# Kernel tuning notes

Hardware: AMD Instinct MI355X
Metric: run time of the kernel (lower is better)

Reference implementation:

```python
import jax, jax.numpy as jnp
import numpy as np

H = 100  # hidden size
T_ENC, T_DEC = 12, 50


def setup_inputs() -> dict:
    key = jax.random.key(0)
    ks = iter(jax.random.split(key, 40))
    n = lambda *s: jax.random.normal(next(ks), s, dtype=jnp.float32) * 0.1
    B = 16384
    inp = {
        "q": jax.random.normal(next(ks), (B, T_ENC, H), dtype=jnp.float32),
        "p": jax.random.normal(next(ks), (B, T_DEC, H), dtype=jnp.float32),
        # attention
        "attn_W": n(H, H), "attn_b": n(H),
        # encoder GRU (2 layers, input 100)
        "eWih0": n(3 * H, H), "eWhh0": n(3 * H, H), "ebih0": n(3 * H), "ebhh0": n(3 * H),
        "eWih1": n(3 * H, H), "eWhh1": n(3 * H, H), "ebih1": n(3 * H), "ebhh1": n(3 * H),
        # decoder GRU (2 layers, layer0 input 200)
        "dWih0": n(3 * H, 2 * H), "dWhh0": n(3 * H, H), "dbih0": n(3 * H), "dbhh0": n(3 * H),
        "dWih1": n(3 * H, H), "dWhh1": n(3 * H, H), "dbih1": n(3 * H), "dbhh1": n(3 * H),
        # out_context Linear(200,50)
        "outW": n(50, 2 * H), "outb": n(50),
        # final MLP 50->25->10->4->2
        "f1W": n(25, 50), "f1b": n(25),
        "f2W": n(10, 25), "f2b": n(10),
        "f3W": n(4, 10), "f3b": n(4),
        "f4W": n(2, 4), "f4b": n(2),
    }
    return inp


def _gru_cell(x, h, Wih, Whh, bih, bhh):
    gi = x @ Wih.T + bih
    gh = h @ Whh.T + bhh
    ir, iz, inn = jnp.split(gi, 3, axis=-1)
    hr, hz, hn = jnp.split(gh, 3, axis=-1)
    r = jax.nn.sigmoid(ir + hr)
    z = jax.nn.sigmoid(iz + hz)
    ng = jnp.tanh(inn + r * hn)
    return (1.0 - z) * ng + z * h


def reference(q, p, attn_W, attn_b,
              eWih0, eWhh0, ebih0, ebhh0, eWih1, eWhh1, ebih1, ebhh1,
              dWih0, dWhh0, dbih0, dbhh0, dWih1, dWhh1, dbih1, dbhh1,
              outW, outb, f1W, f1b, f2W, f2b, f3W, f3b, f4W, f4b):
    B = q.shape[0]
    h_init = jnp.zeros((B, H), q.dtype)

    # encoder: 2-layer GRU over 12 timesteps
    def enc_step(carry, xt):
        h0, h1 = carry
        h0 = _gru_cell(xt, h0, eWih0, eWhh0, ebih0, ebhh0)
        h1 = _gru_cell(h0, h1, eWih1, eWhh1, ebih1, ebhh1)
        return (h0, h1), h1

    (h0, h1), enc_seq = jax.lax.scan(enc_step, (h_init, h_init), jnp.swapaxes(q, 0, 1))
    enc = jnp.swapaxes(enc_seq, 0, 1)  # [B, 12, H]

    # precompute attn energies: Linear(H,H) applied to encoder outputs
    energy = jnp.einsum("btd,ed->bte", enc, attn_W) + attn_b  # [B, 12, H]

    # decoder: 50 steps of attention + 2-layer GRU + out_context
    def dec_step(carry, xt):
        h0, h1 = carry
        scores = jnp.einsum("bd,btd->bt", h1, energy)  # hidden = last layer
        aw = jax.nn.softmax(scores, axis=1)
        ctx = jnp.einsum("bt,btd->bd", aw, enc)  # [B, H]
        gin = jnp.concatenate([xt, ctx], axis=-1)  # [B, 2H]
        h0 = _gru_cell(gin, h0, dWih0, dWhh0, dbih0, dbhh0)
        h1 = _gru_cell(h0, h1, dWih1, dWhh1, dbih1, dbhh1)
        out = jax.nn.relu(jnp.concatenate([h1, ctx], axis=1) @ outW.T + outb)
        return (h0, h1), out

    _, outs = jax.lax.scan(dec_step, (h0, h1), jnp.swapaxes(p, 0, 1))
    s = outs[-1]  # [B, 50]

    s = jax.nn.relu(s @ f1W.T + f1b)
    s = jax.nn.relu(s @ f2W.T + f2b)
    s = jax.nn.relu(s @ f3W.T + f3b)
    return jax.nn.softmax(s @ f4W.T + f4b, axis=1)
```

## Files before the change

### kernel.cpp

```cpp
#include <hip/hip_runtime.h>


#define BB    16384
#define HH    100
#define TE    12
#define TDN   50
#define ROWS  64
#define XS    101
#define GS    205
#define ENCT_OFF 16384

struct Params {
  const float *q, *p, *attn_b;
  const float *eWih0,*eWhh0,*ebih0,*ebhh0,*eWih1,*eWhh1,*ebih1,*ebhh1;
  const float *dWih0,*dWhh0,*dbih0,*dbhh0,*dWih1,*dWhh1,*dbih1,*dbhh1;
  const float *outW,*outb,*f1W,*f1b,*f2W,*f2b,*f3W,*f3b,*f4W,*f4b;
  float *ws;
  float *out;
};

__global__ void prep_attn_t(const float* __restrict__ attn_W, float* __restrict__ ws) {
  int i = blockIdx.x * 256 + threadIdx.x;
  if (i < HH * HH) {
    int d = i / HH, e = i % HH;
    ws[d * HH + e] = attn_W[e * HH + d];
  }
}

__device__ __forceinline__ float sigf(float x)   { return 1.0f / (1.0f + __expf(-x)); }
__device__ __forceinline__ float tanhf_(float x) { float e = __expf(2.0f * x); return 1.0f - 2.0f / (e + 1.0f); }

template<int NG, int K, int LDW>
__device__ __forceinline__ void gemm_sw(const float* __restrict__ W,
                                        const float* xrow, int wv, float* acc) {
  #pragma unroll
  for (int m = 0; m < NG; ++m) acc[m] = 0.0f;
  #pragma unroll 1
  for (int kc = 0; kc < K; kc += 25) {
    float xr[25];
    #pragma unroll
    for (int i = 0; i < 25; ++i) xr[i] = xrow[kc + i];
    #pragma unroll
    for (int m = 0; m < NG; ++m) {
      const float* wr = W + (wv + 4 * m) * LDW + kc;
      float a = acc[m];
      #pragma unroll
      for (int i = 0; i < 25; ++i) a = fmaf(wr[i], xr[i], a);
      acc[m] = a;
    }
  }
}

template<bool WRITE_ENC>
__device__ __forceinline__ void gru_combine(const float* gi, const float* gh,
    const float* __restrict__ bih, const float* __restrict__ bhh,
    int wv, int lane, float (*hS)[XS], float* __restrict__ encT, int grow) {
  #pragma unroll
  for (int m = 0; m < 25; ++m) {
    const int n = wv + 4 * m;
    float ir  = gi[m]      + bih[n];
    float iz  = gi[m + 25] + bih[n + 100];
    float inn = gi[m + 50] + bih[n + 200];
    float hr  = gh[m]      + bhh[n];
    float hz  = gh[m + 25] + bhh[n + 100];
    float hn  = gh[m + 50] + bhh[n + 200];
    float r  = sigf(ir + hr);
    float z  = sigf(iz + hz);
    float ng = tanhf_(inn + r * hn);
    float hp = hS[lane][n];
    float hv = (1.0f - z) * ng + z * hp;
    hS[lane][n] = hv;
    if (WRITE_ENC) encT[n * BB + grow] = hv;
  }
}

__global__ __launch_bounds__(256, 1) void fused_kernel(Params pr) {
  __shared__ float h0s[ROWS][XS];
  __shared__ float h1s[ROWS][XS];
  __shared__ float xb [ROWS][GS];
  __shared__ float gvb[ROWS][XS];
  __shared__ float scb[ROWS][13];
  __shared__ float ob [ROWS][53];

  const int tid  = threadIdx.x;
  const int lane = tid & 63;
  const int wv   = __builtin_amdgcn_readfirstlane(tid >> 6);
  const int r0   = blockIdx.x * ROWS;
  const int grow = r0 + lane;

  for (int it = tid; it < ROWS * XS; it += 256) {
    (&h0s[0][0])[it] = 0.0f;
    (&h1s[0][0])[it] = 0.0f;
  }
  __syncthreads();

  float gi[75], gh[75];

  for (int t = 0; t < TE; ++t) {
    for (int it = tid; it < ROWS * HH; it += 256) {
      int r = it / HH, k = it % HH;
      xb[r][k] = pr.q[(size_t)(r0 + r) * (TE * HH) + t * HH + k];
    }
    __syncthreads();
    gemm_sw<75, 100, 100>(pr.eWih0, &xb[lane][0],  wv, gi);
    gemm_sw<75, 100, 100>(pr.eWhh0, &h0s[lane][0], wv, gh);
    __syncthreads();
    gru_combine<false>(gi, gh, pr.ebih0, pr.ebhh0, wv, lane, h0s, nullptr, grow);
    __syncthreads();
    gemm_sw<75, 100, 100>(pr.eWih1, &h0s[lane][0], wv, gi);
    gemm_sw<75, 100, 100>(pr.eWhh1, &h1s[lane][0], wv, gh);
    __syncthreads();
    gru_combine<true>(gi, gh, pr.ebih1, pr.ebhh1, wv, lane, h1s,
                      pr.ws + ENCT_OFF + (size_t)t * HH * BB, grow);
    __syncthreads();
  }

  const float* encT  = pr.ws + ENCT_OFF;
  const float* attnT = pr.ws;

  for (int t = 0; t < TDN; ++t) {
    {
      float ga[25];
      gemm_sw<25, 100, 100>(attnT, &h1s[lane][0], wv, ga);
      #pragma unroll
      for (int m = 0; m < 25; ++m) gvb[lane][wv + 4 * m] = ga[m];
    }
    float cb = 0.0f;
    #pragma unroll 4
    for (int e = 0; e < HH; ++e) cb = fmaf(h1s[lane][e], pr.attn_b[e], cb);
    __syncthreads();

    {
      const int tb = 3 * wv;
      float sc0 = cb, sc1 = cb, sc2 = cb;
      #pragma unroll 1
      for (int dc = 0; dc < HH; dc += 25) {
        float gv[25];
        #pragma unroll
        for (int i = 0; i < 25; ++i) gv[i] = gvb[lane][dc + i];
        #pragma unroll
        for (int i = 0; i < 25; ++i) {
          sc0 = fmaf(gv[i], encT[(size_t)((tb + 0) * HH + dc + i) * BB + grow], sc0);
          sc1 = fmaf(gv[i], encT[(size_t)((tb + 1) * HH + dc + i) * BB + grow], sc1);
          sc2 = fmaf(gv[i], encT[(size_t)((tb + 2) * HH + dc + i) * BB + grow], sc2);
        }
      }
      scb[lane][tb + 0] = sc0;
      scb[lane][tb + 1] = sc1;
      scb[lane][tb + 2] = sc2;
    }
    __syncthreads();

    float aw[TE];
    {
      float mx = -1e30f;
      #pragma unroll
      for (int k = 0; k < TE; ++k) { float v = scb[lane][k]; aw[k] = v; mx = fmaxf(mx, v); }
      float s = 0.0f;
      #pragma unroll
      for (int k = 0; k < TE; ++k) { float e = __expf(aw[k] - mx); aw[k] = e; s += e; }
      float inv = 1.0f / s;
      #pragma unroll
      for (int k = 0; k < TE; ++k) aw[k] *= inv;
    }

    {
      const int db = 25 * wv;
      float cx[25];
      #pragma unroll
      for (int i = 0; i < 25; ++i) cx[i] = 0.0f;
      #pragma unroll
      for (int k = 0; k < TE; ++k) {
        float a = aw[k];
        #pragma unroll
        for (int i = 0; i < 25; ++i)
          cx[i] = fmaf(a, encT[(size_t)(k * HH + db + i) * BB + grow], cx[i]);
      }
      #pragma unroll
      for (int i = 0; i < 25; ++i) xb[lane][HH + db + i] = cx[i];
    }
    for (int it = tid; it < ROWS * HH; it += 256) {
      int r = it / HH, k = it % HH;
      xb[r][k] = pr.p[(size_t)(r0 + r) * (TDN * HH) + t * HH + k];
    }
    __syncthreads();

    gemm_sw<75, 200, 200>(pr.dWih0, &xb[lane][0],  wv, gi);
    gemm_sw<75, 100, 100>(pr.dWhh0, &h0s[lane][0], wv, gh);
    __syncthreads();
    gru_combine<false>(gi, gh, pr.dbih0, pr.dbhh0, wv, lane, h0s, nullptr, grow);
    __syncthreads();

    gemm_sw<75, 100, 100>(pr.dWih1, &h0s[lane][0], wv, gi);
    gemm_sw<75, 100, 100>(pr.dWhh1, &h1s[lane][0], wv, gh);
    __syncthreads();
    gru_combine<false>(gi, gh, pr.dbih1, pr.dbhh1, wv, lane, h1s, nullptr, grow);
    __syncthreads();
  }

  {
    float acc[13];
    #pragma unroll
    for (int m = 0; m < 13; ++m) acc[m] = 0.0f;
    #pragma unroll 1
    for (int half = 0; half < 2; ++half) {
      const float* xsrc = half ? &xb[lane][HH] : &h1s[lane][0];
      #pragma unroll 1
      for (int kc = 0; kc < HH; kc += 25) {
        float xr[25];
        #pragma unroll
        for (int i = 0; i < 25; ++i) xr[i] = xsrc[kc + i];
        #pragma unroll
        for (int m = 0; m < 13; ++m) {
          const int o = wv + 4 * m;
          if (o < 50) {
            const float* wr = pr.outW + o * 200 + half * HH + kc;
            float a = acc[m];
            #pragma unroll
            for (int i = 0; i < 25; ++i) a = fmaf(wr[i], xr[i], a);
            acc[m] = a;
          }
        }
      }
    }
    #pragma unroll
    for (int m = 0; m < 13; ++m) {
      const int o = wv + 4 * m;
      if (o < 50) ob[lane][o] = fmaxf(acc[m] + pr.outb[o], 0.0f);
    }
  }
  __syncthreads();

  if (wv == 0) {
    float s0[50];
    #pragma unroll
    for (int i = 0; i < 50; ++i) s0[i] = ob[lane][i];
    float s1[25];
    #pragma unroll 1
    for (int o = 0; o < 25; ++o) {
      float a = pr.f1b[o];
      #pragma unroll
      for (int k = 0; k < 50; ++k) a = fmaf(pr.f1W[o * 50 + k], s0[k], a);
      s1[o] = fmaxf(a, 0.0f);
    }
    float s2[10];
    #pragma unroll 1
    for (int o = 0; o < 10; ++o) {
      float a = pr.f2b[o];
      #pragma unroll
      for (int k = 0; k < 25; ++k) a = fmaf(pr.f2W[o * 25 + k], s1[k], a);
      s2[o] = fmaxf(a, 0.0f);
    }
    float s3[4];
    #pragma unroll
    for (int o = 0; o < 4; ++o) {
      float a = pr.f3b[o];
      #pragma unroll
      for (int k = 0; k < 10; ++k) a = fmaf(pr.f3W[o * 10 + k], s2[k], a);
      s3[o] = fmaxf(a, 0.0f);
    }
    float l0 = pr.f4b[0], l1 = pr.f4b[1];
    #pragma unroll
    for (int k = 0; k < 4; ++k) {
      l0 = fmaf(pr.f4W[k],     s3[k], l0);
      l1 = fmaf(pr.f4W[4 + k], s3[k], l1);
    }
    float mx = fmaxf(l0, l1);
    float e0 = __expf(l0 - mx), e1 = __expf(l1 - mx);
    float inv = 1.0f / (e0 + e1);
    pr.out[(size_t)grow * 2 + 0] = e0 * inv;
    pr.out[(size_t)grow * 2 + 1] = e1 * inv;
  }
}

extern "C" void kernel_launch(void* const* d_in, const int* in_sizes, int n_in,
                              void* d_out, int out_size, void* d_ws, size_t ws_size,
                              hipStream_t stream) {
  Params pr;
  pr.q      = (const float*)d_in[0];
  pr.p      = (const float*)d_in[1];
  pr.attn_b = (const float*)d_in[3];
  pr.eWih0  = (const float*)d_in[4];
  pr.eWhh0  = (const float*)d_in[5];
  pr.ebih0  = (const float*)d_in[6];
  pr.ebhh0  = (const float*)d_in[7];
  pr.eWih1  = (const float*)d_in[8];
  pr.eWhh1  = (const float*)d_in[9];
  pr.ebih1  = (const float*)d_in[10];
  pr.ebhh1  = (const float*)d_in[11];
  pr.dWih0  = (const float*)d_in[12];
  pr.dWhh0  = (const float*)d_in[13];
  pr.dbih0  = (const float*)d_in[14];
  pr.dbhh0  = (const float*)d_in[15];
  pr.dWih1  = (const float*)d_in[16];
  pr.dWhh1  = (const float*)d_in[17];
  pr.dbih1  = (const float*)d_in[18];
  pr.dbhh1  = (const float*)d_in[19];
  pr.outW   = (const float*)d_in[20];
  pr.outb   = (const float*)d_in[21];
  pr.f1W    = (const float*)d_in[22];
  pr.f1b    = (const float*)d_in[23];
  pr.f2W    = (const float*)d_in[24];
  pr.f2b    = (const float*)d_in[25];
  pr.f3W    = (const float*)d_in[26];
  pr.f3b    = (const float*)d_in[27];
  pr.f4W    = (const float*)d_in[28];
  pr.f4b    = (const float*)d_in[29];
  pr.ws     = (float*)d_ws;
  pr.out    = (float*)d_out;

  prep_attn_t<<<40, 256, 0, stream>>>((const float*)d_in[2], (float*)d_ws);
  fused_kernel<<<BB / ROWS, 256, 0, stream>>>(pr);
}
```

Baseline: 31.96 ms.

## Split K across wave halves, shrink rows per block, raise occupancy

Each block now handles 32 rows with 512 threads. Each wave splits the reduction dimension in two halves across lanes 0-31 and 32-63 and combines them with a cross-lane shuffle. The GRU gate GEMMs and the combine step are fused into one per-cell routine that works on small register blocks, which lowers register pressure so the launch bounds can request 4 blocks per CU. The attention-bias dot product is dropped because a constant added to every score cancels in the softmax, and the softmax normalisation is folded into the context write. The cost is extra shuffles, half-idle lanes during writeback, and more repeated weight reads per row.

```diff
diff --git a/kernel.cpp b/kernel.cpp
--- a/kernel.cpp
+++ b/kernel.cpp
@@ -5,13 +5,14 @@
 #define HH    100
 #define TE    12
 #define TDN   50
-#define ROWS  64
+#define ROWS  32
+#define NT    512
 #define XS    101
 #define GS    205
 #define ENCT_OFF 16384
 
 struct Params {
-  const float *q, *p, *attn_b;
+  const float *q, *p;
   const float *eWih0,*eWhh0,*ebih0,*ebhh0,*eWih1,*eWhh1,*ebih1,*ebhh1;
   const float *dWih0,*dWhh0,*dbih0,*dbhh0,*dWih1,*dWhh1,*dbih1,*dbhh1;
   const float *outW,*outb,*f1W,*f1b,*f2W,*f2b,*f3W,*f3b,*f4W,*f4b;
@@ -30,51 +31,93 @@
 __device__ __forceinline__ float sigf(float x)   { return 1.0f / (1.0f + __expf(-x)); }
 __device__ __forceinline__ float tanhf_(float x) { float e = __expf(2.0f * x); return 1.0f - 2.0f / (e + 1.0f); }
 
-template<int NG, int K, int LDW>
-__device__ __forceinline__ void gemm_sw(const float* __restrict__ W,
-                                        const float* xrow, int wv, float* acc) {
+template<int KI>
+__device__ __forceinline__ void gru_cell_g8(
+    const float* __restrict__ Wih, const float* __restrict__ Whh,
+    const float* __restrict__ bih, const float* __restrict__ bhh,
+    const float* xrow, const float* hrow, int wv, int kh, float* hv)
+{
+  constexpr int KH = KI / 2;
+  const float* xh   = xrow + kh * KH;
+  const float* hsrc = hrow + kh * 50;
   #pragma unroll
-  for (int m = 0; m < NG; ++m) acc[m] = 0.0f;
-  #pragma unroll 1
-  for (int kc = 0; kc < K; kc += 25) {
-    float xr[25];
-    #pragma unroll
-    for (int i = 0; i < 25; ++i) xr[i] = xrow[kc + i];
-    #pragma unroll
-    for (int m = 0; m < NG; ++m) {
-      const float* wr = W + (wv + 4 * m) * LDW + kc;
-      float a = acc[m];
-      #pragma unroll
-      for (int i = 0; i < 25; ++i) a = fmaf(wr[i], xr[i], a);
-      acc[m] = a;
+  for (int b = 0; b < 2; ++b) {
+    const int MC = b ? 6 : 7;
+    float gi[21], gh[21];
+    #pragma unroll
+    for (int i = 0; i < 21; ++i) { gi[i] = 0.f; gh[i] = 0.f; }
+    #pragma unroll 1
+    for (int kc = 0; kc < KH; kc += 10) {
+      float xr[10];
+      #pragma unroll
+      for (int i = 0; i < 10; ++i) xr[i] = xh[kc + i];
+      #pragma unroll
+      for (int mm = 0; mm < 7; ++mm) {
+        if (mm < MC) {
+          const int n = 8 * (7 * b + mm) + wv;
+          if (b == 0 || mm < 5 || n < HH) {
+            #pragma unroll
+            for (int g = 0; g < 3; ++g) {
+              const float* wr = Wih + (size_t)(n + g * HH) * KI + kh * KH + kc;
+              float a = gi[3 * mm + g];
+              #pragma unroll
+              for (int i = 0; i < 10; ++i) a = fmaf(wr[i], xr[i], a);
+              gi[3 * mm + g] = a;
+            }
+          }
+        }
+      }
+    }
+    #pragma unroll 1
+    for (int kc = 0; kc < 50; kc += 10) {
+      float xr[10];
+      #pragma unroll
+      for (int i = 0; i < 10; ++i) xr[i] = hsrc[kc + i];
+      #pragma unroll
+      for (int mm = 0; mm < 7; ++mm) {
+        if (mm < MC) {
+          const int n = 8 * (7 * b + mm) + wv;
+          if (b == 0 || mm < 5 || n < HH) {
+            #pragma unroll
+            for (int g = 0; g < 3; ++g) {
+              const float* wr = Whh + (size_t)(n + g * HH) * HH + kh * 50 + kc;
+              float a = gh[3 * mm + g];
+              #pragma unroll
+              for (int i = 0; i < 10; ++i) a = fmaf(wr[i], xr[i], a);
+              gh[3 * mm + g] = a;
+            }
+          }
+        }
+      }
+    }
+    #pragma unroll
+    for (int i = 0; i < 21; ++i) {
+      gi[i] += __shfl_xor(gi[i], 32);
+      gh[i] += __shfl_xor(gh[i], 32);
+    }
+    #pragma unroll
+    for (int mm = 0; mm < 7; ++mm) {
+      if (mm < MC) {
+        const int m = 7 * b + mm;
+        const int n = 8 * m + wv;
+        if (b == 0 || mm < 5 || n < HH) {
+          float ir  = gi[3 * mm + 0] + bih[n];
+          float iz  = gi[3 * mm + 1] + bih[n + HH];
+          float in_ = gi[3 * mm + 2] + bih[n + 2 * HH];
+          float hr  = gh[3 * mm + 0] + bhh[n];
+          float hz  = gh[3 * mm + 1] + bhh[n + HH];
+          float hn  = gh[3 * mm + 2] + bhh[n + 2 * HH];
+          float r  = sigf(ir + hr);
+          float z  = sigf(iz + hz);
+          float ng = tanhf_(in_ + r * hn);
+          hv[m] = (1.0f - z) * ng + z * hrow[n];
+        }
+      }
     }
   }
 }
 
-template<bool WRITE_ENC>
-__device__ __forceinline__ void gru_combine(const float* gi, const float* gh,
-    const float* __restrict__ bih, const float* __restrict__ bhh,
-    int wv, int lane, float (*hS)[XS], float* __restrict__ encT, int grow) {
-  #pragma unroll
-  for (int m = 0; m < 25; ++m) {
-    const int n = wv + 4 * m;
-    float ir  = gi[m]      + bih[n];
-    float iz  = gi[m + 25] + bih[n + 100];
-    float inn = gi[m + 50] + bih[n + 200];
-    float hr  = gh[m]      + bhh[n];
-    float hz  = gh[m + 25] + bhh[n + 100];
-    float hn  = gh[m + 50] + bhh[n + 200];
-    float r  = sigf(ir + hr);
-    float z  = sigf(iz + hz);
-    float ng = tanhf_(inn + r * hn);
-    float hp = hS[lane][n];
-    float hv = (1.0f - z) * ng + z * hp;
-    hS[lane][n] = hv;
-    if (WRITE_ENC) encT[n * BB + grow] = hv;
-  }
-}
-
-__global__ __launch_bounds__(256, 1) void fused_kernel(Params pr) {
+__global__ __launch_bounds__(NT, 4) void fused_kernel(Params pr) {
   __shared__ float h0s[ROWS][XS];
   __shared__ float h1s[ROWS][XS];
   __shared__ float xb [ROWS][GS];
@@ -84,164 +127,189 @@
 
   const int tid  = threadIdx.x;
   const int lane = tid & 63;
+  const int row  = lane & 31;
+  const int kh   = lane >> 5;
   const int wv   = __builtin_amdgcn_readfirstlane(tid >> 6);
   const int r0   = blockIdx.x * ROWS;
-  const int grow = r0 + lane;
-
-  for (int it = tid; it < ROWS * XS; it += 256) {
-    (&h0s[0][0])[it] = 0.0f;
-    (&h1s[0][0])[it] = 0.0f;
+  const int grow = r0 + row;
+
+  for (int it = tid; it < ROWS * XS; it += NT) {
+    (&h0s[0][0])[it] = 0.f;
+    (&h1s[0][0])[it] = 0.f;
   }
   __syncthreads();
 
-  float gi[75], gh[75];
+  float hv[13];
+  float*       encT  = pr.ws + ENCT_OFF;
+  const float* attnT = pr.ws;
 
   for (int t = 0; t < TE; ++t) {
-    for (int it = tid; it < ROWS * HH; it += 256) {
+    for (int it = tid; it < ROWS * HH; it += NT) {
       int r = it / HH, k = it % HH;
       xb[r][k] = pr.q[(size_t)(r0 + r) * (TE * HH) + t * HH + k];
     }
     __syncthreads();
-    gemm_sw<75, 100, 100>(pr.eWih0, &xb[lane][0],  wv, gi);
-    gemm_sw<75, 100, 100>(pr.eWhh0, &h0s[lane][0], wv, gh);
-    __syncthreads();
-    gru_combine<false>(gi, gh, pr.ebih0, pr.ebhh0, wv, lane, h0s, nullptr, grow);
-    __syncthreads();
-    gemm_sw<75, 100, 100>(pr.eWih1, &h0s[lane][0], wv, gi);
-    gemm_sw<75, 100, 100>(pr.eWhh1, &h1s[lane][0], wv, gh);
-    __syncthreads();
-    gru_combine<true>(gi, gh, pr.ebih1, pr.ebhh1, wv, lane, h1s,
-                      pr.ws + ENCT_OFF + (size_t)t * HH * BB, grow);
-    __syncthreads();
-  }
-
-  const float* encT  = pr.ws + ENCT_OFF;
-  const float* attnT = pr.ws;
+    gru_cell_g8<100>(pr.eWih0, pr.eWhh0, pr.ebih0, pr.ebhh0,
+                     &xb[row][0], &h0s[row][0], wv, kh, hv);
+    __syncthreads();
+    if (lane < 32) {
+      #pragma unroll
+      for (int m = 0; m < 13; ++m) { int n = 8 * m + wv; if (n < HH) h0s[row][n] = hv[m]; }
+    }
+    __syncthreads();
+    gru_cell_g8<100>(pr.eWih1, pr.eWhh1, pr.ebih1, pr.ebhh1,
+                     &h0s[row][0], &h1s[row][0], wv, kh, hv);
+    __syncthreads();
+    if (lane < 32) {
+      float* ep = encT + (size_t)t * HH * BB;
+      #pragma unroll
+      for (int m = 0; m < 13; ++m) {
+        int n = 8 * m + wv;
+        if (n < HH) { h1s[row][n] = hv[m]; ep[(size_t)n * BB + grow] = hv[m]; }
+      }
+    }
+    __syncthreads();
+  }
 
   for (int t = 0; t < TDN; ++t) {
     {
-      float ga[25];
-      gemm_sw<25, 100, 100>(attnT, &h1s[lane][0], wv, ga);
-      #pragma unroll
-      for (int m = 0; m < 25; ++m) gvb[lane][wv + 4 * m] = ga[m];
-    }
-    float cb = 0.0f;
-    #pragma unroll 4
-    for (int e = 0; e < HH; ++e) cb = fmaf(h1s[lane][e], pr.attn_b[e], cb);
+      float ga[13];
+      #pragma unroll
+      for (int m = 0; m < 13; ++m) ga[m] = 0.f;
+      const float* hsrc = &h1s[row][0] + kh * 50;
+      #pragma unroll 1
+      for (int kc = 0; kc < 50; kc += 10) {
+        float xr[10];
+        #pragma unroll
+        for (int i = 0; i < 10; ++i) xr[i] = hsrc[kc + i];
+        #pragma unroll
+        for (int m = 0; m < 13; ++m) {
+          const int d = 8 * m + wv;
+          if (m < 12 || d < HH) {
+            const float* wr = attnT + (size_t)d * HH + kh * 50 + kc;
+            float a = ga[m];
+            #pragma unroll
+            for (int i = 0; i < 10; ++i) a = fmaf(wr[i], xr[i], a);
+            ga[m] = a;
+          }
+        }
+      }
+      #pragma unroll
+      for (int m = 0; m < 13; ++m) ga[m] += __shfl_xor(ga[m], 32);
+      if (lane < 32) {
+        #pragma unroll
+        for (int m = 0; m < 13; ++m) { int d = 8 * m + wv; if (d < HH) gvb[row][d] = ga[m]; }
+      }
+    }
     __syncthreads();
 
     {
-      const int tb = 3 * wv;
-      float sc0 = cb, sc1 = cb, sc2 = cb;
-      #pragma unroll 1
-      for (int dc = 0; dc < HH; dc += 25) {
-        float gv[25];
+      const int ts = wv * 2 + kh;
+      if (ts < TE) {
+        float s = 0.f;
+        const float* ep = encT + (size_t)ts * HH * BB + grow;
+        #pragma unroll 1
+        for (int kc = 0; kc < HH; kc += 10) {
+          #pragma unroll
+          for (int i = 0; i < 10; ++i)
+            s = fmaf(gvb[row][kc + i], ep[(size_t)(kc + i) * BB], s);
+        }
+        scb[row][ts] = s;
+      }
+    }
+    __syncthreads();
+
+    {
+      const int ds = wv * 2 + kh;
+      const int d0 = ds < 4 ? ds * 7 : 28 + (ds - 4) * 6;
+      const int dc = ds < 4 ? 7 : 6;
+      float aw[TE]; float mx = -1e30f;
+      #pragma unroll
+      for (int k = 0; k < TE; ++k) { float v = scb[row][k]; aw[k] = v; mx = fmaxf(mx, v); }
+      float ssum = 0.f;
+      #pragma unroll
+      for (int k = 0; k < TE; ++k) { float e = __expf(aw[k] - mx); aw[k] = e; ssum += e; }
+      const float inv = 1.0f / ssum;
+      float cx[7];
+      #pragma unroll
+      for (int i = 0; i < 7; ++i) cx[i] = 0.f;
+      #pragma unroll
+      for (int k = 0; k < TE; ++k) {
+        const float* ep = encT + (size_t)(k * HH + d0) * BB + grow;
+        const float a = aw[k];
         #pragma unroll
-        for (int i = 0; i < 25; ++i) gv[i] = gvb[lane][dc + i];
-        #pragma unroll
-        for (int i = 0; i < 25; ++i) {
-          sc0 = fmaf(gv[i], encT[(size_t)((tb + 0) * HH + dc + i) * BB + grow], sc0);
-          sc1 = fmaf(gv[i], encT[(size_t)((tb + 1) * HH + dc + i) * BB + grow], sc1);
-          sc2 = fmaf(gv[i], encT[(size_t)((tb + 2) * HH + dc + i) * BB + grow], sc2);
-        }
-      }
-      scb[lane][tb + 0] = sc0;
-      scb[lane][tb + 1] = sc1;
-      scb[lane][tb + 2] = sc2;
-    }
-    __syncthreads();
-
-    float aw[TE];
-    {
-      float mx = -1e30f;
-      #pragma unroll
-      for (int k = 0; k < TE; ++k) { float v = scb[lane][k]; aw[k] = v; mx = fmaxf(mx, v); }
-      float s = 0.0f;
-      #pragma unroll
-      for (int k = 0; k < TE; ++k) { float e = __expf(aw[k] - mx); aw[k] = e; s += e; }
-      float inv = 1.0f / s;
-      #pragma unroll
-      for (int k = 0; k < TE; ++k) aw[k] *= inv;
-    }
-
-    {
-      const int db = 25 * wv;
-      float cx[25];
-      #pragma unroll
-      for (int i = 0; i < 25; ++i) cx[i] = 0.0f;
-      #pragma unroll
-      for (int k = 0; k < TE; ++k) {
-        float a = aw[k];
-        #pragma unroll
-        for (int i = 0; i < 25; ++i)
-          cx[i] = fmaf(a, encT[(size_t)(k * HH + db + i) * BB + grow], cx[i]);
-      }
-      #pragma unroll
-      for (int i = 0; i < 25; ++i) xb[lane][HH + db + i] = cx[i];
-    }
-    for (int it = tid; it < ROWS * HH; it += 256) {
+        for (int i = 0; i < 7; ++i) if (i < dc) cx[i] = fmaf(a, ep[(size_t)i * BB], cx[i]);
+      }
+      #pragma unroll
+      for (int i = 0; i < 7; ++i) if (i < dc) xb[row][HH + d0 + i] = cx[i] * inv;
+    }
+    for (int it = tid; it < ROWS * HH; it += NT) {
       int r = it / HH, k = it % HH;
       xb[r][k] = pr.p[(size_t)(r0 + r) * (TDN * HH) + t * HH + k];
     }
     __syncthreads();
 
-    gemm_sw<75, 200, 200>(pr.dWih0, &xb[lane][0],  wv, gi);
-    gemm_sw<75, 100, 100>(pr.dWhh0, &h0s[lane][0], wv, gh);
-    __syncthreads();
-    gru_combine<false>(gi, gh, pr.dbih0, pr.dbhh0, wv, lane, h0s, nullptr, grow);
-    __syncthreads();
-
-    gemm_sw<75, 100, 100>(pr.dWih1, &h0s[lane][0], wv, gi);
-    gemm_sw<75, 100, 100>(pr.dWhh1, &h1s[lane][0], wv, gh);
-    __syncthreads();
-    gru_combine<false>(gi, gh, pr.dbih1, pr.dbhh1, wv, lane, h1s, nullptr, grow);
+    gru_cell_g8<200>(pr.dWih0, pr.dWhh0, pr.dbih0, pr.dbhh0,
+                     &xb[row][0], &h0s[row][0], wv, kh, hv);
+    __syncthreads();
+    if (lane < 32) {
+      #pragma unroll
+      for (int m = 0; m < 13; ++m) { int n = 8 * m + wv; if (n < HH) h0s[row][n] = hv[m]; }
+    }
+    __syncthreads();
+
+    gru_cell_g8<100>(pr.dWih1, pr.dWhh1, pr.dbih1, pr.dbhh1,
+                     &h0s[row][0], &h1s[row][0], wv, kh, hv);
+    __syncthreads();
+    if (lane < 32) {
+      #pragma unroll
+      for (int m = 0; m < 13; ++m) { int n = 8 * m + wv; if (n < HH) h1s[row][n] = hv[m]; }
+    }
     __syncthreads();
   }
 
   {
-    float acc[13];
-    #pragma unroll
-    for (int m = 0; m < 13; ++m) acc[m] = 0.0f;
-    #pragma unroll 1
-    for (int half = 0; half < 2; ++half) {
-      const float* xsrc = half ? &xb[lane][HH] : &h1s[lane][0];
-      #pragma unroll 1
-      for (int kc = 0; kc < HH; kc += 25) {
-        float xr[25];
-        #pragma unroll
-        for (int i = 0; i < 25; ++i) xr[i] = xsrc[kc + i];
-        #pragma unroll
-        for (int m = 0; m < 13; ++m) {
-          const int o = wv + 4 * m;
-          if (o < 50) {
-            const float* wr = pr.outW + o * 200 + half * HH + kc;
-            float a = acc[m];
-            #pragma unroll
-            for (int i = 0; i < 25; ++i) a = fmaf(wr[i], xr[i], a);
-            acc[m] = a;
-          }
-        }
-      }
-    }
-    #pragma unroll
-    for (int m = 0; m < 13; ++m) {
-      const int o = wv + 4 * m;
-      if (o < 50) ob[lane][o] = fmaxf(acc[m] + pr.outb[o], 0.0f);
+    float oa[7];
+    #pragma unroll
+    for (int i = 0; i < 7; ++i) oa[i] = 0.f;
+    const int OC = (wv < 2) ? 7 : 6;
+    const float* xsrc = kh ? &xb[row][HH] : &h1s[row][0];
+    #pragma unroll 1
+    for (int kc = 0; kc < HH; kc += 10) {
+      float xr[10];
+      #pragma unroll
+      for (int i = 0; i < 10; ++i) xr[i] = xsrc[kc + i];
+      #pragma unroll
+      for (int mm = 0; mm < 7; ++mm) {
+        if (mm < OC) {
+          const int o = 8 * mm + wv;
+          const float* wr = pr.outW + (size_t)o * (2 * HH) + kh * HH + kc;
+          float a = oa[mm];
+          #pragma unroll
+          for (int i = 0; i < 10; ++i) a = fmaf(wr[i], xr[i], a);
+          oa[mm] = a;
+        }
+      }
+    }
+    #pragma unroll
+    for (int i = 0; i < 7; ++i) oa[i] += __shfl_xor(oa[i], 32);
+    if (lane < 32) {
+      #pragma unroll
+      for (int mm = 0; mm < 7; ++mm) {
+        if (mm < OC) { int o = 8 * mm + wv; ob[row][o] = fmaxf(oa[mm] + pr.outb[o], 0.f); }
+      }
     }
   }
   __syncthreads();
 
-  if (wv == 0) {
-    float s0[50];
-    #pragma unroll
-    for (int i = 0; i < 50; ++i) s0[i] = ob[lane][i];
+  if (wv == 0 && lane < 32) {
     float s1[25];
     #pragma unroll 1
     for (int o = 0; o < 25; ++o) {
       float a = pr.f1b[o];
       #pragma unroll
-      for (int k = 0; k < 50; ++k) a = fmaf(pr.f1W[o * 50 + k], s0[k], a);
-      s1[o] = fmaxf(a, 0.0f);
+      for (int k = 0; k < 50; ++k) a = fmaf(pr.f1W[o * 50 + k], ob[row][k], a);
+      s1[o] = fmaxf(a, 0.f);
     }
     float s2[10];
     #pragma unroll 1
@@ -249,7 +317,7 @@
       float a = pr.f2b[o];
       #pragma unroll
       for (int k = 0; k < 25; ++k) a = fmaf(pr.f2W[o * 25 + k], s1[k], a);
-      s2[o] = fmaxf(a, 0.0f);
+      s2[o] = fmaxf(a, 0.f);
     }
     float s3[4];
     #pragma unroll
@@ -257,7 +325,7 @@
       float a = pr.f3b[o];
       #pragma unroll
       for (int k = 0; k < 10; ++k) a = fmaf(pr.f3W[o * 10 + k], s2[k], a);
-      s3[o] = fmaxf(a, 0.0f);
+      s3[o] = fmaxf(a, 0.f);
     }
     float l0 = pr.f4b[0], l1 = pr.f4b[1];
     #pragma unroll
@@ -279,7 +347,6 @@
   Params pr;
   pr.q      = (const float*)d_in[0];
   pr.p      = (const float*)d_in[1];
-  pr.attn_b = (const float*)d_in[3];
   pr.eWih0  = (const float*)d_in[4];
   pr.eWhh0  = (const float*)d_in[5];
   pr.ebih0  = (const float*)d_in[6];
@@ -310,5 +377,5 @@
   pr.out    = (float*)d_out;
 
   prep_attn_t<<<40, 256, 0, stream>>>((const float*)d_in[2], (float*)d_ws);
-  fused_kernel<<<BB / ROWS, 256, 0, stream>>>(pr);
+  fused_kernel<<<BB / ROWS, NT, 0, stream>>>(pr);
 }
```

Result: slower. 53.06 ms (+66.0%).
